# Performance work log

Measured on AMD Instinct MI355X. Metric: run time of the kernel, lower is better.

The kernel has to match this reference:

```python
import jax, jax.numpy as jnp
import numpy as np

NUM_HEADS = 16


def setup_inputs() -> dict:
    rng = jax.random.key(0)
    ks = jax.random.split(rng, 11)
    T, B, E = 1024, 4, 1024
    s = E ** -0.5  # weight init scale
    return {
        "query": jax.random.normal(ks[0], (T, B, E), jnp.float32),
        "key": jax.random.normal(ks[1], (T, B, E), jnp.float32),
        "value": jax.random.normal(ks[2], (T, B, E), jnp.float32),
        "q_proj_weight": jax.random.normal(ks[3], (E, E), jnp.float32) * s,
        "k_proj_weight1": jax.random.normal(ks[4], (E, E), jnp.float32) * s,
        "k_proj_weight2": jax.random.normal(ks[5], (E, E), jnp.float32) * s,
        "v_proj_weight": jax.random.normal(ks[6], (E, E), jnp.float32) * s,
        "in_proj_bias": jax.random.normal(ks[7], (4 * E,), jnp.float32) * 0.02,
        "out_proj_weight": jax.random.normal(ks[8], (E, E), jnp.float32) * s,
        "out_proj_bias": jax.random.normal(ks[9], (E,), jnp.float32) * 0.02,
        "pi": jax.random.uniform(ks[10], (2, NUM_HEADS), jnp.float32, 0.3, 0.7),
    }


def reference(query, key, value, q_proj_weight, k_proj_weight1, k_proj_weight2,
              v_proj_weight, in_proj_bias, out_proj_weight, out_proj_bias, pi):
    T, Bz, E = query.shape
    H = NUM_HEADS
    hd = E // H
    scaling = hd ** -0.5

    b_q, b_k1, b_k2, b_v = jnp.split(in_proj_bias, 4)
    q = query @ q_proj_weight.T + b_q
    k1 = key @ k_proj_weight1.T + b_k1
    k2 = key @ k_proj_weight2.T + b_k2
    v = value @ v_proj_weight.T + b_v

    def heads(x):  # (S, B, E) -> (B*H, S, hd)
        S = x.shape[0]
        return x.reshape(S, Bz * H, hd).transpose(1, 0, 2)

    q, k1, k2, v = heads(q), heads(k1), heads(k2), heads(v)

    def sqdist(a, b):  # (B*H, Nt, hd), (B*H, Ns, hd) -> (B*H, Nt, Ns)
        a2 = jnp.sum(a * a, axis=-1)
        b2 = jnp.sum(b * b, axis=-1)
        ab = jnp.einsum('btd,bsd->bts', a, b)
        return a2[:, :, None] + b2[:, None, :] - 2.0 * ab

    e1 = jnp.exp(-scaling / 2.0 * sqdist(q, k1))
    e2 = jnp.exp(-3.0 * scaling / 2.0 * sqdist(q, k2))

    pi1 = jnp.clip(jnp.abs(pi[0]), 1e-6, 2.0)  # (H,)
    pi2 = jnp.clip(jnp.abs(pi[1]), 1e-6, 2.0)

    Nt, Ns = e1.shape[1], e1.shape[2]
    attn = (e1.reshape(Bz, H, Nt, Ns) * pi1[None, :, None, None]
            + e2.reshape(Bz, H, Nt, Ns) * pi2[None, :, None, None])
    attn = attn.reshape(Bz * H, Nt, Ns)
    attn = attn / (jnp.sum(attn, axis=-1, keepdims=True) + 1e-6)

    out = jnp.einsum('bts,bsd->btd', attn, v)        # (B*H, Nt, hd)
    out = out.transpose(1, 0, 2).reshape(T, Bz, E)   # (T, B, E)
    return out @ out_proj_weight.T + out_proj_bias
```

## Files before the change

### kernel.cpp

```cpp
#include <hip/hip_runtime.h>
#include <hip/hip_bf16.h>

#define T_DIM 1024
#define B_DIM 4
#define E_DIM 1024
#define H_DIM 16
#define HD    64
#define M_DIM (T_DIM * B_DIM)

typedef __hip_bfloat16 bf16;
typedef __bf16 bf16x8 __attribute__((ext_vector_type(8)));
typedef __bf16 bf16x4 __attribute__((ext_vector_type(4)));
typedef float  f32x4  __attribute__((ext_vector_type(4)));

#define P4S ((size_t)M_DIM * E_DIM)
#define P1S ((size_t)E_DIM * E_DIM)

__global__ __launch_bounds__(256) void cvt_all(
    const float* __restrict__ q, const float* __restrict__ k,
    const float* __restrict__ v, const float* __restrict__ w0,
    const float* __restrict__ w1, const float* __restrict__ w2,
    const float* __restrict__ w3, const float* __restrict__ w4,
    __bf16* __restrict__ dst)
{
  size_t i = ((size_t)blockIdx.x * 256 + threadIdx.x) * 8;
  const float* src;
  size_t off;
  if (i < P4S)            { src = q; off = i; }
  else if (i < 2 * P4S)   { src = k; off = i - P4S; }
  else if (i < 3 * P4S)   { src = v; off = i - 2 * P4S; }
  else {
    size_t j = i - 3 * P4S;
    int wsel = (int)(j >> 20);
    off = j & (P1S - 1);
    const float* ws[5] = {w0, w1, w2, w3, w4};
    src = ws[wsel];
  }
  float4 a = *(const float4*)(src + off);
  float4 b = *(const float4*)(src + off + 4);
  bf16x8 o;
  o[0] = (__bf16)a.x; o[1] = (__bf16)a.y; o[2] = (__bf16)a.z; o[3] = (__bf16)a.w;
  o[4] = (__bf16)b.x; o[5] = (__bf16)b.y; o[6] = (__bf16)b.z; o[7] = (__bf16)b.w;
  *(bf16x8*)(dst + i) = o;
}

__device__ __forceinline__ void load_lds16(const __bf16* g, __bf16* l) {
  __builtin_amdgcn_global_load_lds(
      (__attribute__((address_space(1))) void*)(void*)g,
      (__attribute__((address_space(3))) void*)l, 16, 0, 0);
}

__device__ __forceinline__ void stage_half(
    int H, const __bf16* __restrict__ X, const __bf16* __restrict__ W,
    int bm, int bn, __bf16* As, __bf16* Bs, int tid)
{
  if (H >= 64) return;
  const int T  = H >> 2;
  const int h  = H & 3;
  const int rh = (h & 1) * 128;
  const __bf16* src = (h < 2) ? X : W;
  const int rbase   = (h < 2) ? bm : bn;
  __bf16* lb = ((h < 2) ? As : Bs) + (T & 1) * 16384;
#pragma unroll
  for (int li = 0; li < 2; ++li) {
    int r  = rh + li * 64 + (tid >> 3);
    int gc = (tid & 7) ^ (r & 7);
    load_lds16(src + (size_t)(rbase + r) * E_DIM + T * 64 + gc * 8,
               lb + (rh + li * 64) * 64 + tid * 8);
  }
}

#define RD(base, row, c) \
  (*(const bf16x8*)((base) + (row) * 64 + ((((c) ^ ((row) & 7))) << 3)))

__global__ __launch_bounds__(512, 2) void proj_gemm4(
    const __bf16* __restrict__ xbase, const __bf16* __restrict__ wbase,
    const float* __restrict__ bin, __bf16* __restrict__ cbase)
{
  __shared__ __bf16 lds[65536];
  __bf16* As = lds;
  __bf16* Bs = lds + 32768;

  const int z = blockIdx.z;
  const __bf16* X = xbase + ((z == 0) ? 0 : (z == 3) ? 2 * P4S : P4S);
  const __bf16* W = wbase + (size_t)z * P1S;
  const float* bias = bin + z * E_DIM;
  __bf16* C = cbase + (size_t)z * P4S;

  const int bm = blockIdx.x * 256;
  const int bn = blockIdx.y * 256;

  const int tid  = threadIdx.x;
  const int lane = tid & 63;
  const int w    = tid >> 6;
  const int wm   = w >> 2;
  const int wn   = w & 3;
  const int mrow = lane & 15, quad = lane >> 4;

  f32x4 acc[8][4];
#pragma unroll
  for (int m = 0; m < 8; ++m)
#pragma unroll
    for (int n = 0; n < 4; ++n) acc[m][n] = (f32x4)0.0f;

#pragma unroll
  for (int H = 0; H < 5; ++H) stage_half(H, X, W, bm, bn, As, Bs, tid);
  asm volatile("s_waitcnt vmcnt(2)" ::: "memory");
  __builtin_amdgcn_s_barrier();

  bf16x8 af[4][2];
  bf16x8 bq[4][2];

#pragma unroll 2
  for (int t = 0; t < 16; ++t) {
    const __bf16* Ab = As + (t & 1) * 16384;
    const __bf16* Bb = Bs + (t & 1) * 16384;

#pragma unroll
    for (int n = 0; n < 2; ++n)
#pragma unroll
      for (int kk = 0; kk < 2; ++kk)
        bq[n][kk] = RD(Bb, wn * 64 + n * 16 + mrow, kk * 4 + quad);
#pragma unroll
    for (int m = 0; m < 4; ++m)
#pragma unroll
      for (int kk = 0; kk < 2; ++kk)
        af[m][kk] = RD(Ab, wm * 128 + m * 16 + mrow, kk * 4 + quad);
    stage_half(4 * t + 5, X, W, bm, bn, As, Bs, tid);
    __builtin_amdgcn_s_barrier();
    asm volatile("s_waitcnt lgkmcnt(0)" ::: "memory");
    __builtin_amdgcn_s_setprio(1);
#pragma unroll
    for (int kk = 0; kk < 2; ++kk)
#pragma unroll
      for (int n = 0; n < 2; ++n)
#pragma unroll
        for (int m = 0; m < 4; ++m)
          acc[m][n] = __builtin_amdgcn_mfma_f32_16x16x32_bf16(
              af[m][kk], bq[n][kk], acc[m][n], 0, 0, 0);
    __builtin_amdgcn_s_setprio(0);
    __builtin_amdgcn_s_barrier();

#pragma unroll
    for (int n = 2; n < 4; ++n)
#pragma unroll
      for (int kk = 0; kk < 2; ++kk)
        bq[n][kk] = RD(Bb, wn * 64 + n * 16 + mrow, kk * 4 + quad);
    stage_half(4 * t + 6, X, W, bm, bn, As, Bs, tid);
    __builtin_amdgcn_s_barrier();
    asm volatile("s_waitcnt lgkmcnt(0)" ::: "memory");
    __builtin_amdgcn_s_setprio(1);
#pragma unroll
    for (int kk = 0; kk < 2; ++kk)
#pragma unroll
      for (int n = 2; n < 4; ++n)
#pragma unroll
        for (int m = 0; m < 4; ++m)
          acc[m][n] = __builtin_amdgcn_mfma_f32_16x16x32_bf16(
              af[m][kk], bq[n][kk], acc[m][n], 0, 0, 0);
    __builtin_amdgcn_s_setprio(0);
    __builtin_amdgcn_s_barrier();

#pragma unroll
    for (int m = 0; m < 4; ++m)
#pragma unroll
      for (int kk = 0; kk < 2; ++kk)
        af[m][kk] = RD(Ab, wm * 128 + 64 + m * 16 + mrow, kk * 4 + quad);
    stage_half(4 * t + 7, X, W, bm, bn, As, Bs, tid);
    __builtin_amdgcn_s_barrier();
    asm volatile("s_waitcnt lgkmcnt(0)" ::: "memory");
    __builtin_amdgcn_s_setprio(1);
#pragma unroll
    for (int kk = 0; kk < 2; ++kk)
#pragma unroll
      for (int n = 0; n < 2; ++n)
#pragma unroll
        for (int m = 0; m < 4; ++m)
          acc[4 + m][n] = __builtin_amdgcn_mfma_f32_16x16x32_bf16(
              af[m][kk], bq[n][kk], acc[4 + m][n], 0, 0, 0);
    __builtin_amdgcn_s_setprio(0);
    __builtin_amdgcn_s_barrier();

    stage_half(4 * t + 8, X, W, bm, bn, As, Bs, tid);
    __builtin_amdgcn_s_barrier();
    __builtin_amdgcn_s_setprio(1);
#pragma unroll
    for (int kk = 0; kk < 2; ++kk)
#pragma unroll
      for (int n = 2; n < 4; ++n)
#pragma unroll
        for (int m = 0; m < 4; ++m)
          acc[4 + m][n] = __builtin_amdgcn_mfma_f32_16x16x32_bf16(
              af[m][kk], bq[n][kk], acc[4 + m][n], 0, 0, 0);
    __builtin_amdgcn_s_setprio(0);
    if (t < 14)       { asm volatile("s_waitcnt vmcnt(2)" ::: "memory"); }
    else if (t == 14) { asm volatile("s_waitcnt vmcnt(0)" ::: "memory"); }
    __builtin_amdgcn_s_barrier();
  }

#pragma unroll
  for (int n = 0; n < 4; ++n) {
    int col = bn + wn * 64 + n * 16 + mrow;
    float bc = bias[col];
#pragma unroll
    for (int m = 0; m < 8; ++m) {
      int rbase = bm + wm * 128 + m * 16 + quad * 4;
#pragma unroll
      for (int r = 0; r < 4; ++r)
        C[(size_t)(rbase + r) * E_DIM + col] = (__bf16)(acc[m][n][r] + bc);
    }
  }
}

template <typename TO>
__device__ __forceinline__ void gemm_body(
    const __bf16* __restrict__ X, const __bf16* __restrict__ W,
    const float* __restrict__ bias, TO* __restrict__ C,
    int bm, int bn, int Ndim, int Kdim, __bf16* As, __bf16* Bs)
{
  const int tid  = threadIdx.x;
  const int lane = tid & 63;
  const int wave = tid >> 6;
  const int wy = (wave >> 1) * 64;
  const int wx = (wave & 1) * 64;
  const int mrow = lane & 15, quad = lane >> 4;

  const int srow = tid >> 2;
  const int ke   = (tid & 3) * 8;
  const __bf16* gA0 = X + (size_t)(bm + srow)      * Kdim + ke;
  const __bf16* gA1 = X + (size_t)(bm + srow + 64) * Kdim + ke;
  const __bf16* gB0 = W + (size_t)(bn + srow)      * Kdim + ke;
  const __bf16* gB1 = W + (size_t)(bn + srow + 64) * Kdim + ke;
  __bf16* lA0 = As + tid * 8;
  __bf16* lA1 = As + (tid + 256) * 8;
  __bf16* lB0 = Bs + tid * 8;
  __bf16* lB1 = Bs + (tid + 256) * 8;

  f32x4 acc[4][4];
#pragma unroll
  for (int i = 0; i < 4; ++i)
#pragma unroll
    for (int j = 0; j < 4; ++j) acc[i][j] = (f32x4)0.0f;

  for (int k0 = 0; k0 < Kdim; k0 += 32) {
    __syncthreads();
    load_lds16(gA0 + k0, lA0);
    load_lds16(gA1 + k0, lA1);
    load_lds16(gB0 + k0, lB0);
    load_lds16(gB1 + k0, lB1);
    __syncthreads();
    bf16x8 af[4], bf[4];
#pragma unroll
    for (int i = 0; i < 4; ++i)
      af[i] = *(const bf16x8*)(As + (wy + i * 16 + mrow) * 32 + quad * 8);
#pragma unroll
    for (int j = 0; j < 4; ++j)
      bf[j] = *(const bf16x8*)(Bs + (wx + j * 16 + mrow) * 32 + quad * 8);
#pragma unroll
    for (int i = 0; i < 4; ++i)
#pragma unroll
      for (int j = 0; j < 4; ++j)
        acc[i][j] = __builtin_amdgcn_mfma_f32_16x16x32_bf16(af[i], bf[j], acc[i][j], 0, 0, 0);
  }

#pragma unroll
  for (int j = 0; j < 4; ++j) {
    int col = bn + wx + j * 16 + mrow;
    float bc = bias[col];
#pragma unroll
    for (int i = 0; i < 4; ++i) {
      int rbase = bm + wy + i * 16 + quad * 4;
#pragma unroll
      for (int r = 0; r < 4; ++r)
        C[(size_t)(rbase + r) * Ndim + col] = (TO)(acc[i][j][r] + bc);
    }
  }
}

__global__ __launch_bounds__(256) void out_gemm(
    const __bf16* __restrict__ X, const __bf16* __restrict__ W,
    const float* __restrict__ bias, float* __restrict__ C)
{
  __shared__ __bf16 As[128 * 32];
  __shared__ __bf16 Bs[128 * 32];
  gemm_body<float>(X, W, bias, C, blockIdx.x * 128, blockIdx.y * 128,
                   E_DIM, E_DIM, As, Bs);
}

__global__ __launch_bounds__(256) void norms_vt(
    const __bf16* __restrict__ Qp, const __bf16* __restrict__ K1p,
    const __bf16* __restrict__ K2p, const __bf16* __restrict__ Vp,
    float* __restrict__ qn, float* __restrict__ kn1, float* __restrict__ kn2,
    __bf16* __restrict__ Vt_g)
{
  __shared__ __bf16 tile[64][88];
  const int tid = threadIdx.x;
  if (blockIdx.x < 768) {
    int id = blockIdx.x * 256 + tid;
    int which = id >> 16;
    int r = id & 65535;
    int bh = r >> 10, t = r & 1023;
    int b = bh >> 4, h = bh & 15;
    const __bf16* src = (which == 0) ? Qp : ((which == 1) ? K1p : K2p);
    float* dst = (which == 0) ? qn : ((which == 1) ? kn1 : kn2);
    const __bf16* p = src + (size_t)(t * 4 + b) * 1024 + h * 64;
    float s = 0.f;
#pragma unroll
    for (int c = 0; c < 8; ++c) {
      bf16x8 v = *(const bf16x8*)(p + c * 8);
#pragma unroll
      for (int j = 0; j < 8; ++j) { float x = (float)v[j]; s += x * x; }
    }
    dst[bh * 1024 + t] = s;
    return;
  }
  int bid = blockIdx.x - 768;
  const int bh = bid & 63, kt = bid >> 6;
  const int b = bh >> 4, h = bh & 15;
  {
    int s = tid >> 2, d0 = (tid & 3) * 16;
    const __bf16* src = Vp + (size_t)((kt * 64 + s) * 4 + b) * 1024 + h * 64 + d0;
    *(bf16x8*)(&tile[s][d0])     = *(const bf16x8*)(src);
    *(bf16x8*)(&tile[s][d0 + 8]) = *(const bf16x8*)(src + 8);
  }
  __syncthreads();
#pragma unroll
  for (int c = 0; c < 2; ++c) {
    int idx = tid * 2 + c;
    int d = idx >> 3, u0 = (idx & 7) * 8;
    bf16x8 o;
#pragma unroll
    for (int i = 0; i < 8; ++i) {
      int u = u0 + i;
      int s = (u & 3) * 16 + (u >> 2);
      o[i] = tile[s][d];
    }
    *(bf16x8*)(Vt_g + ((size_t)bh * 64 + d) * 1024 + kt * 64 + u0) = o;
  }
}

__global__ __launch_bounds__(512, 4) void mgk_attn_mfma(
    const __bf16* __restrict__ Qp, const __bf16* __restrict__ K1p,
    const __bf16* __restrict__ K2p, const __bf16* __restrict__ Vt_g,
    const float* __restrict__ qn_g, const float* __restrict__ kn1_g,
    const float* __restrict__ kn2_g, const float* __restrict__ pi,
    __bf16* __restrict__ AO)
{
  __shared__ __bf16 lds[32768];
  __bf16* Pl = lds + 24576;

  const int bh = blockIdx.x, qt = blockIdx.y;
  const int b = bh >> 4, h = bh & 15;
  const int tid = threadIdx.x, lane = tid & 63, w = tid >> 6;
  const int mrow = lane & 15, quad = lane >> 4;

  const float cl1 = 0.0625f * 1.4426950408889634f;
  const float cl2 = 0.1875f * 1.4426950408889634f;
  const float L1 = 2.0f * cl1, L2 = 2.0f * cl2;
  const float p1 = fminf(fmaxf(fabsf(pi[h]), 1e-6f), 2.0f);
  const float p2 = fminf(fmaxf(fabsf(pi[H_DIM + h]), 1e-6f), 2.0f);
  const float lp1 = __log2f(p1), lp2 = __log2f(p2);
  const int hoff = h * 64;

  bf16x8 af[2];
  {
    const __bf16* qp = Qp + (size_t)((qt * 128 + w * 16 + mrow) * 4 + b) * 1024
                       + hoff + quad * 8;
    af[0] = *(const bf16x8*)(qp);
    af[1] = *(const bf16x8*)(qp + 32);
  }
  f32x4 qnv = *(const f32x4*)(qn_g + bh * 1024 + qt * 128 + w * 16 + quad * 4);
  f32x4 aq2;
#pragma unroll
  for (int r = 0; r < 4; ++r) aq2[r] = fmaf(cl1 - cl2, qnv[r], lp2);

  const int srow = tid >> 3;
  const int sc   = tid & 7;
  const int gc   = sc ^ (srow & 7);
  const int doff = tid * 8;
  const __bf16* gK1 = K1p + (size_t)(srow * 4 + b) * 1024 + hoff + gc * 8;
  const __bf16* gK2 = K2p + (size_t)(srow * 4 + b) * 1024 + hoff + gc * 8;
  const __bf16* gVt = Vt_g + ((size_t)bh * 64 + srow) * 1024 + gc * 8;

#define STAGE_T(kt_, bsel_) do {                                         \
    __bf16* bb_ = lds + (bsel_) * 12288;                                 \
    load_lds16(gK1 + (size_t)(kt_) * 262144, bb_ + doff);                \
    load_lds16(gK2 + (size_t)(kt_) * 262144, bb_ + 4096 + doff);         \
    load_lds16(gVt + (kt_) * 64,             bb_ + 8192 + doff);         \
  } while (0)

  STAGE_T(0, 0);
  STAGE_T(1, 1);
  asm volatile("s_waitcnt vmcnt(3)" ::: "memory");
  __builtin_amdgcn_s_barrier();
  asm volatile("" ::: "memory");

  f32x4 oacc[4];
#pragma unroll
  for (int j = 0; j < 4; ++j) oacc[j] = (f32x4)0.0f;
  f32x4 rsl = (f32x4)0.0f;

  for (int kt = 0; kt < 16; ++kt) {
    const int cur = kt & 1;
    const __bf16* K1s = lds + cur * 12288;
    const __bf16* K2s = K1s + 4096;
    const __bf16* Vt  = K1s + 8192;

    float nb1[4], s2[4];
#pragma unroll
    for (int j = 0; j < 4; ++j) {
      float f1 = kn1_g[bh * 1024 + kt * 64 + j * 16 + mrow];
      float f2 = kn2_g[bh * 1024 + kt * 64 + j * 16 + mrow];
      nb1[j] = fmaf(-cl1, f1, lp1);
      s2[j]  = -cl2 * f2;
    }

    f32x4 acc1[4], acc2[4];
#pragma unroll
    for (int j = 0; j < 4; ++j) { acc1[j] = (f32x4)0.0f; acc2[j] = (f32x4)0.0f; }
    __builtin_amdgcn_s_setprio(1);
#pragma unroll
    for (int kk = 0; kk < 2; ++kk)
#pragma unroll
      for (int j = 0; j < 4; ++j) {
        bf16x8 b1f = *(const bf16x8*)(K1s + (j * 16 + mrow) * 64
                                      + (((kk * 4 + quad) ^ (mrow & 7)) << 3));
        bf16x8 b2f = *(const bf16x8*)(K2s + (j * 16 + mrow) * 64
                                      + (((kk * 4 + quad) ^ (mrow & 7)) << 3));
        acc1[j] = __builtin_amdgcn_mfma_f32_16x16x32_bf16(af[kk], b1f, acc1[j], 0, 0, 0);
        acc2[j] = __builtin_amdgcn_mfma_f32_16x16x32_bf16(af[kk], b2f, acc2[j], 0, 0, 0);
      }
    __builtin_amdgcn_s_setprio(0);

    f32x4 pv[4];
#pragma unroll
    for (int j = 0; j < 4; ++j) {
      f32x4 p;
#pragma unroll
      for (int r = 0; r < 4; ++r) {
        float e1 = __builtin_amdgcn_exp2f(fmaf(L1, acc1[j][r], nb1[j]));
        float e2 = __builtin_amdgcn_exp2f(fmaf(L2, acc2[j][r], s2[j] + aq2[r]));
        p[r] = e1 + e2;
      }
      pv[j] = p;
      rsl += p;
    }
#pragma unroll
    for (int r = 0; r < 4; ++r) {
      int q = quad * 4 + r;
      bf16x4 pk;
      pk[0] = (__bf16)pv[0][r]; pk[1] = (__bf16)pv[1][r];
      pk[2] = (__bf16)pv[2][r]; pk[3] = (__bf16)pv[3][r];
      int lc = mrow >> 1;
      *(bf16x4*)(Pl + w * 1024 + q * 64 + ((lc ^ (q & 7)) << 3) + (mrow & 1) * 4) = pk;
    }

    bf16x8 pf[2];
#pragma unroll
    for (int kk = 0; kk < 2; ++kk)
      pf[kk] = *(const bf16x8*)(Pl + w * 1024 + mrow * 64
                                + (((kk * 4 + quad) ^ (mrow & 7)) << 3));
    __builtin_amdgcn_s_setprio(1);
#pragma unroll
    for (int kk = 0; kk < 2; ++kk)
#pragma unroll
      for (int j = 0; j < 4; ++j) {
        bf16x8 vf = *(const bf16x8*)(Vt + (j * 16 + mrow) * 64
                                     + (((kk * 4 + quad) ^ (mrow & 7)) << 3));
        oacc[j] = __builtin_amdgcn_mfma_f32_16x16x32_bf16(pf[kk], vf, oacc[j], 0, 0, 0);
      }
    __builtin_amdgcn_s_setprio(0);

    if (kt < 15) {
      asm volatile("s_waitcnt lgkmcnt(0)" ::: "memory");
      __builtin_amdgcn_s_barrier();
      if (kt < 14) {
        STAGE_T(kt + 2, cur);
        asm volatile("s_waitcnt vmcnt(3)" ::: "memory");
      } else {
        asm volatile("s_waitcnt vmcnt(0)" ::: "memory");
      }
      __builtin_amdgcn_s_barrier();
      asm volatile("" ::: "memory");
    }
  }
#undef STAGE_T

#pragma unroll
  for (int d = 1; d < 16; d <<= 1) {
    f32x4 o;
#pragma unroll
    for (int r = 0; r < 4; ++r) o[r] = __shfl_xor(rsl[r], d, 64);
    rsl += o;
  }

  f32x4 inv;
#pragma unroll
  for (int r = 0; r < 4; ++r) inv[r] = 1.0f / (rsl[r] + 1e-6f);
#pragma unroll
  for (int j = 0; j < 4; ++j) {
    int col = hoff + j * 16 + mrow;
#pragma unroll
    for (int r = 0; r < 4; ++r) {
      int t = qt * 128 + w * 16 + quad * 4 + r;
      AO[(size_t)(t * 4 + b) * 1024 + col] = (__bf16)(oacc[j][r] * inv[r]);
    }
  }
}

extern "C" void kernel_launch(void* const* d_in, const int* in_sizes, int n_in,
                              void* d_out, int out_size, void* d_ws, size_t ws_size,
                              hipStream_t stream) {
  const float* query = (const float*)d_in[0];
  const float* key   = (const float*)d_in[1];
  const float* value = (const float*)d_in[2];
  const float* Wq    = (const float*)d_in[3];
  const float* Wk1   = (const float*)d_in[4];
  const float* Wk2   = (const float*)d_in[5];
  const float* Wv    = (const float*)d_in[6];
  const float* bin   = (const float*)d_in[7];
  const float* Wo    = (const float*)d_in[8];
  const float* bo    = (const float*)d_in[9];
  const float* pi    = (const float*)d_in[10];
  float* out = (float*)d_out;

  __bf16* qc  = (__bf16*)d_ws;
  __bf16* wq  = qc  + 3 * P4S;
  __bf16* wo  = wq  + 4 * P1S;
  __bf16* Qp  = wq  + 5 * P1S;
  __bf16* K1p = Qp  + P4S;
  __bf16* K2p = K1p + P4S;
  __bf16* Vp  = K2p + P4S;
  __bf16* AO  = Vp  + P4S;
  float*  qn_g  = (float*)(AO + P4S);
  float*  kn1_g = qn_g  + 64 * 1024;
  float*  kn2_g = kn1_g + 64 * 1024;
  __bf16* Vt_g  = qc;

  cvt_all<<<8704, 256, 0, stream>>>(query, key, value, Wq, Wk1, Wk2, Wv, Wo, qc);

  proj_gemm4<<<dim3(M_DIM / 256, E_DIM / 256, 4), 512, 0, stream>>>(qc, wq, bin, Qp);

  norms_vt<<<768 + 1024, 256, 0, stream>>>(Qp, K1p, K2p, Vp,
                                           qn_g, kn1_g, kn2_g, Vt_g);

  mgk_attn_mfma<<<dim3(64, 8), 512, 0, stream>>>(
      Qp, K1p, K2p, Vt_g, qn_g, kn1_g, kn2_g, pi, AO);

  out_gemm<<<dim3(M_DIM / 128, E_DIM / 128), 256, 0, stream>>>(AO, wo, bo, out);
}
```

Measured before the change: 238.3 us.

## Give each attention wave two query row tiles and preload key norms into LDS

```diff
diff --git a/kernel.cpp b/kernel.cpp
--- a/kernel.cpp
+++ b/kernel.cpp
@@ -49,6 +49,11 @@
       (__attribute__((address_space(1))) void*)(void*)g,
       (__attribute__((address_space(3))) void*)l, 16, 0, 0);
 }
+__device__ __forceinline__ void load_lds4(const float* g, float* l) {
+  __builtin_amdgcn_global_load_lds(
+      (__attribute__((address_space(1))) void*)(void*)g,
+      (__attribute__((address_space(3))) void*)l, 4, 0, 0);
+}
 
 __device__ __forceinline__ void stage_half(
     int H, const __bf16* __restrict__ X, const __bf16* __restrict__ W,
@@ -339,17 +344,22 @@
   }
 }
 
-__global__ __launch_bounds__(512, 4) void mgk_attn_mfma(
+__global__ __launch_bounds__(256, 2) void mgk_attn_mfma(
     const __bf16* __restrict__ Qp, const __bf16* __restrict__ K1p,
     const __bf16* __restrict__ K2p, const __bf16* __restrict__ Vt_g,
     const float* __restrict__ qn_g, const float* __restrict__ kn1_g,
     const float* __restrict__ kn2_g, const float* __restrict__ pi,
     __bf16* __restrict__ AO)
 {
-  __shared__ __bf16 lds[32768];
+  __shared__ __bf16 lds[36864];
   __bf16* Pl = lds + 24576;
-
-  const int bh = blockIdx.x, qt = blockIdx.y;
+  float* knl1 = (float*)(lds + 32768);
+  float* knl2 = knl1 + 1024;
+
+  const int bid = blockIdx.x;
+  const int mm  = bid >> 3;
+  const int bh  = (bid & 7) * 8 + (mm & 7);
+  const int qt  = mm >> 3;
   const int b = bh >> 4, h = bh & 15;
   const int tid = threadIdx.x, lane = tid & 63, w = tid >> 6;
   const int mrow = lane & 15, quad = lane >> 4;
@@ -362,43 +372,51 @@
   const float lp1 = __log2f(p1), lp2 = __log2f(p2);
   const int hoff = h * 64;
 
-  bf16x8 af[2];
-  {
-    const __bf16* qp = Qp + (size_t)((qt * 128 + w * 16 + mrow) * 4 + b) * 1024
+  bf16x8 af[2][2];
+  f32x4 aq2[2];
+#pragma unroll
+  for (int m = 0; m < 2; ++m) {
+    const __bf16* qp = Qp + (size_t)((qt * 128 + w * 32 + m * 16 + mrow) * 4 + b) * 1024
                        + hoff + quad * 8;
-    af[0] = *(const bf16x8*)(qp);
-    af[1] = *(const bf16x8*)(qp + 32);
-  }
-  f32x4 qnv = *(const f32x4*)(qn_g + bh * 1024 + qt * 128 + w * 16 + quad * 4);
-  f32x4 aq2;
-#pragma unroll
-  for (int r = 0; r < 4; ++r) aq2[r] = fmaf(cl1 - cl2, qnv[r], lp2);
-
-  const int srow = tid >> 3;
-  const int sc   = tid & 7;
-  const int gc   = sc ^ (srow & 7);
-  const int doff = tid * 8;
-  const __bf16* gK1 = K1p + (size_t)(srow * 4 + b) * 1024 + hoff + gc * 8;
-  const __bf16* gK2 = K2p + (size_t)(srow * 4 + b) * 1024 + hoff + gc * 8;
-  const __bf16* gVt = Vt_g + ((size_t)bh * 64 + srow) * 1024 + gc * 8;
-
-#define STAGE_T(kt_, bsel_) do {                                         \
-    __bf16* bb_ = lds + (bsel_) * 12288;                                 \
-    load_lds16(gK1 + (size_t)(kt_) * 262144, bb_ + doff);                \
-    load_lds16(gK2 + (size_t)(kt_) * 262144, bb_ + 4096 + doff);         \
-    load_lds16(gVt + (kt_) * 64,             bb_ + 8192 + doff);         \
+    af[m][0] = *(const bf16x8*)(qp);
+    af[m][1] = *(const bf16x8*)(qp + 32);
+    f32x4 qnv = *(const f32x4*)(qn_g + bh * 1024 + qt * 128 + w * 32 + m * 16 + quad * 4);
+#pragma unroll
+    for (int r = 0; r < 4; ++r) aq2[m][r] = fmaf(cl1 - cl2, qnv[r], lp2);
+  }
+
+#pragma unroll
+  for (int i = 0; i < 4; ++i) {
+    load_lds4(kn1_g + bh * 1024 + i * 256 + tid, knl1 + i * 256 + tid);
+    load_lds4(kn2_g + bh * 1024 + i * 256 + tid, knl2 + i * 256 + tid);
+  }
+
+#define STAGE_T(kt_, bsel_) do {                                              \
+    __bf16* bb_ = lds + (bsel_) * 12288;                                      \
+    _Pragma("unroll")                                                         \
+    for (int li_ = 0; li_ < 2; ++li_) {                                       \
+      int idx_ = li_ * 256 + tid;                                             \
+      int row_ = idx_ >> 3;                                                   \
+      int gc_  = (idx_ & 7) ^ (row_ & 7);                                     \
+      size_t krow_ = (size_t)(((kt_) * 64 + row_) * 4 + b) * 1024 + hoff + gc_ * 8; \
+      load_lds16(K1p + krow_, bb_ + idx_ * 8);                                \
+      load_lds16(K2p + krow_, bb_ + 4096 + idx_ * 8);                         \
+      load_lds16(Vt_g + ((size_t)bh * 64 + row_) * 1024 + (kt_) * 64 + gc_ * 8, \
+                 bb_ + 8192 + idx_ * 8);                                      \
+    }                                                                         \
   } while (0)
 
   STAGE_T(0, 0);
   STAGE_T(1, 1);
-  asm volatile("s_waitcnt vmcnt(3)" ::: "memory");
+  asm volatile("s_waitcnt vmcnt(6)" ::: "memory");
   __builtin_amdgcn_s_barrier();
-  asm volatile("" ::: "memory");
-
-  f32x4 oacc[4];
-#pragma unroll
-  for (int j = 0; j < 4; ++j) oacc[j] = (f32x4)0.0f;
-  f32x4 rsl = (f32x4)0.0f;
+
+  f32x4 oacc[2][4];
+#pragma unroll
+  for (int m = 0; m < 2; ++m)
+#pragma unroll
+    for (int j = 0; j < 4; ++j) oacc[m][j] = (f32x4)0.0f;
+  f32x4 rsl[2] = {(f32x4)0.0f, (f32x4)0.0f};
 
   for (int kt = 0; kt < 16; ++kt) {
     const int cur = kt & 1;
@@ -406,18 +424,18 @@
     const __bf16* K2s = K1s + 4096;
     const __bf16* Vt  = K1s + 8192;
 
-    float nb1[4], s2[4];
+    float f1[4], f2[4];
 #pragma unroll
     for (int j = 0; j < 4; ++j) {
-      float f1 = kn1_g[bh * 1024 + kt * 64 + j * 16 + mrow];
-      float f2 = kn2_g[bh * 1024 + kt * 64 + j * 16 + mrow];
-      nb1[j] = fmaf(-cl1, f1, lp1);
-      s2[j]  = -cl2 * f2;
-    }
-
-    f32x4 acc1[4], acc2[4];
-#pragma unroll
-    for (int j = 0; j < 4; ++j) { acc1[j] = (f32x4)0.0f; acc2[j] = (f32x4)0.0f; }
+      f1[j] = knl1[kt * 64 + j * 16 + mrow];
+      f2[j] = knl2[kt * 64 + j * 16 + mrow];
+    }
+
+    f32x4 acc1[2][4], acc2[2][4];
+#pragma unroll
+    for (int m = 0; m < 2; ++m)
+#pragma unroll
+      for (int j = 0; j < 4; ++j) { acc1[m][j] = (f32x4)0.0f; acc2[m][j] = (f32x4)0.0f; }
     __builtin_amdgcn_s_setprio(1);
 #pragma unroll
     for (int kk = 0; kk < 2; ++kk)
@@ -427,39 +445,53 @@
                                       + (((kk * 4 + quad) ^ (mrow & 7)) << 3));
         bf16x8 b2f = *(const bf16x8*)(K2s + (j * 16 + mrow) * 64
                                       + (((kk * 4 + quad) ^ (mrow & 7)) << 3));
-        acc1[j] = __builtin_amdgcn_mfma_f32_16x16x32_bf16(af[kk], b1f, acc1[j], 0, 0, 0);
-        acc2[j] = __builtin_amdgcn_mfma_f32_16x16x32_bf16(af[kk], b2f, acc2[j], 0, 0, 0);
+#pragma unroll
+        for (int m = 0; m < 2; ++m) {
+          acc1[m][j] = __builtin_amdgcn_mfma_f32_16x16x32_bf16(af[m][kk], b1f, acc1[m][j], 0, 0, 0);
+          acc2[m][j] = __builtin_amdgcn_mfma_f32_16x16x32_bf16(af[m][kk], b2f, acc2[m][j], 0, 0, 0);
+        }
       }
     __builtin_amdgcn_s_setprio(0);
 
-    f32x4 pv[4];
+    float nb1[4], s2[4];
 #pragma unroll
     for (int j = 0; j < 4; ++j) {
-      f32x4 p;
+      nb1[j] = fmaf(-cl1, f1[j], lp1);
+      s2[j]  = -cl2 * f2[j];
+    }
+#pragma unroll
+    for (int m = 0; m < 2; ++m) {
+      f32x4 pv[4];
+#pragma unroll
+      for (int j = 0; j < 4; ++j) {
+        f32x4 p;
+#pragma unroll
+        for (int r = 0; r < 4; ++r) {
+          float e1 = __builtin_amdgcn_exp2f(fmaf(L1, acc1[m][j][r], nb1[j]));
+          float e2 = __builtin_amdgcn_exp2f(fmaf(L2, acc2[m][j][r], s2[j] + aq2[m][r]));
+          p[r] = e1 + e2;
+        }
+        pv[j] = p;
+        rsl[m] += p;
+      }
 #pragma unroll
       for (int r = 0; r < 4; ++r) {
-        float e1 = __builtin_amdgcn_exp2f(fmaf(L1, acc1[j][r], nb1[j]));
-        float e2 = __builtin_amdgcn_exp2f(fmaf(L2, acc2[j][r], s2[j] + aq2[r]));
-        p[r] = e1 + e2;
+        int q = m * 16 + quad * 4 + r;
+        bf16x4 pk;
+        pk[0] = (__bf16)pv[0][r]; pk[1] = (__bf16)pv[1][r];
+        pk[2] = (__bf16)pv[2][r]; pk[3] = (__bf16)pv[3][r];
+        int lc = mrow >> 1;
+        *(bf16x4*)(Pl + w * 2048 + q * 64 + ((lc ^ (q & 7)) << 3) + (mrow & 1) * 4) = pk;
       }
-      pv[j] = p;
-      rsl += p;
-    }
-#pragma unroll
-    for (int r = 0; r < 4; ++r) {
-      int q = quad * 4 + r;
-      bf16x4 pk;
-      pk[0] = (__bf16)pv[0][r]; pk[1] = (__bf16)pv[1][r];
-      pk[2] = (__bf16)pv[2][r]; pk[3] = (__bf16)pv[3][r];
-      int lc = mrow >> 1;
-      *(bf16x4*)(Pl + w * 1024 + q * 64 + ((lc ^ (q & 7)) << 3) + (mrow & 1) * 4) = pk;
-    }
-
-    bf16x8 pf[2];
-#pragma unroll
-    for (int kk = 0; kk < 2; ++kk)
-      pf[kk] = *(const bf16x8*)(Pl + w * 1024 + mrow * 64
-                                + (((kk * 4 + quad) ^ (mrow & 7)) << 3));
+    }
+
+    bf16x8 pf[2][2];
+#pragma unroll
+    for (int m = 0; m < 2; ++m)
+#pragma unroll
+      for (int kk = 0; kk < 2; ++kk)
+        pf[m][kk] = *(const bf16x8*)(Pl + w * 2048 + (m * 16 + mrow) * 64
+                                     + (((kk * 4 + quad) ^ (mrow & 7)) << 3));
     __builtin_amdgcn_s_setprio(1);
 #pragma unroll
     for (int kk = 0; kk < 2; ++kk)
@@ -467,7 +499,9 @@
       for (int j = 0; j < 4; ++j) {
         bf16x8 vf = *(const bf16x8*)(Vt + (j * 16 + mrow) * 64
                                      + (((kk * 4 + quad) ^ (mrow & 7)) << 3));
-        oacc[j] = __builtin_amdgcn_mfma_f32_16x16x32_bf16(pf[kk], vf, oacc[j], 0, 0, 0);
+#pragma unroll
+        for (int m = 0; m < 2; ++m)
+          oacc[m][j] = __builtin_amdgcn_mfma_f32_16x16x32_bf16(pf[m][kk], vf, oacc[m][j], 0, 0, 0);
       }
     __builtin_amdgcn_s_setprio(0);
 
@@ -476,7 +510,7 @@
       __builtin_amdgcn_s_barrier();
       if (kt < 14) {
         STAGE_T(kt + 2, cur);
-        asm volatile("s_waitcnt vmcnt(3)" ::: "memory");
+        asm volatile("s_waitcnt vmcnt(6)" ::: "memory");
       } else {
         asm volatile("s_waitcnt vmcnt(0)" ::: "memory");
       }
@@ -487,23 +521,25 @@
 #undef STAGE_T
 
 #pragma unroll
-  for (int d = 1; d < 16; d <<= 1) {
-    f32x4 o;
-#pragma unroll
-    for (int r = 0; r < 4; ++r) o[r] = __shfl_xor(rsl[r], d, 64);
-    rsl += o;
-  }
-
-  f32x4 inv;
-#pragma unroll
-  for (int r = 0; r < 4; ++r) inv[r] = 1.0f / (rsl[r] + 1e-6f);
-#pragma unroll
-  for (int j = 0; j < 4; ++j) {
-    int col = hoff + j * 16 + mrow;
-#pragma unroll
-    for (int r = 0; r < 4; ++r) {
-      int t = qt * 128 + w * 16 + quad * 4 + r;
-      AO[(size_t)(t * 4 + b) * 1024 + col] = (__bf16)(oacc[j][r] * inv[r]);
+  for (int m = 0; m < 2; ++m) {
+#pragma unroll
+    for (int d = 1; d < 16; d <<= 1) {
+      f32x4 o;
+#pragma unroll
+      for (int r = 0; r < 4; ++r) o[r] = __shfl_xor(rsl[m][r], d, 64);
+      rsl[m] += o;
+    }
+    f32x4 inv;
+#pragma unroll
+    for (int r = 0; r < 4; ++r) inv[r] = 1.0f / (rsl[m][r] + 1e-6f);
+#pragma unroll
+    for (int j = 0; j < 4; ++j) {
+      int col = hoff + j * 16 + mrow;
+#pragma unroll
+      for (int r = 0; r < 4; ++r) {
+        int t = qt * 128 + w * 32 + m * 16 + quad * 4 + r;
+        AO[(size_t)(t * 4 + b) * 1024 + col] = (__bf16)(oacc[m][j][r] * inv[r]);
+      }
     }
   }
 }
@@ -544,7 +580,7 @@
   norms_vt<<<768 + 1024, 256, 0, stream>>>(Qp, K1p, K2p, Vp,
                                            qn_g, kn1_g, kn2_g, Vt_g);
 
-  mgk_attn_mfma<<<dim3(64, 8), 512, 0, stream>>>(
+  mgk_attn_mfma<<<512, 256, 0, stream>>>(
       Qp, K1p, K2p, Vt_g, qn_g, kn1_g, kn2_g, pi, AO);
 
   out_gemm<<<dim3(M_DIM / 128, E_DIM / 128), 256, 0, stream>>>(AO, wo, bo, out);
```

New measurement: 239.5 us. About the same (+0.5%).
